# Optimization experiments

Hardware: AMD Instinct MI355X
Metric: run time of the kernel (lower is better)

The kernel has to match this reference:

```python
import jax, jax.numpy as jnp
import numpy as np

N, E, G = 100000, 1600000, 64
IN, H, OUT = 128, 64, 16  # hidden/2 = 32
SLOPE = 0.01


def setup_inputs() -> dict:
    key = jax.random.key(0)
    ks = jax.random.split(key, 7)
    features = jax.random.normal(ks[0], (N, IN), dtype=jnp.float32)
    src = jax.random.randint(ks[1], (E,), 0, N)
    dst = jax.random.randint(ks[2], (E,), 0, N)
    graph_ids = jnp.sort(jax.random.randint(ks[3], (N,), 0, G))
    # kaiming-uniform-ish fan_in init, bias=False everywhere
    W1 = jax.random.uniform(ks[4], (IN, H), jnp.float32, -1.0, 1.0) * np.sqrt(3.0 / IN)
    W2 = jax.random.uniform(ks[5], (H, H // 2), jnp.float32, -1.0, 1.0) * np.sqrt(3.0 / H)
    Wc = jax.random.uniform(ks[6], (H // 2, OUT), jnp.float32, -1.0, 1.0) * np.sqrt(3.0 / (H // 2))
    return {"features": features, "src": src, "dst": dst, "graph_ids": graph_ids,
            "W1": W1, "W2": W2, "Wc": Wc}


def _graph_conv(x, W, src, dst, n):
    # DGL GraphConv, norm='both', bias=False:
    # out = D_in^{-1/2} A (D_out^{-1/2} x) W   (degrees clamped to >= 1)
    ones = jnp.ones(src.shape[0], dtype=x.dtype)
    outdeg = jnp.clip(jax.ops.segment_sum(ones, src, num_segments=n), 1.0)
    indeg = jnp.clip(jax.ops.segment_sum(ones, dst, num_segments=n), 1.0)
    h = (x * jax.lax.rsqrt(outdeg)[:, None]) @ W  # project first (in_dim > out_dim)
    m = jax.ops.segment_sum(h[src], dst, num_segments=n)  # sparse aggregation
    return m * jax.lax.rsqrt(indeg)[:, None]


def reference(features, src, dst, graph_ids, W1, W2, Wc):
    h = jax.nn.leaky_relu(_graph_conv(features, W1, src, dst, N), SLOPE)
    h = jax.nn.leaky_relu(_graph_conv(h, W2, src, dst, N), SLOPE)
    # dropout is identity at inference
    sums = jax.ops.segment_sum(h, graph_ids, num_segments=G)
    cnts = jnp.clip(jax.ops.segment_sum(jnp.ones((N,), h.dtype), graph_ids, num_segments=G), 1.0)
    mean = sums / cnts[:, None]  # dgl.mean_nodes
    return mean @ Wc  # [G, OUT]
```

## Files before the change

kernel.cpp:

```cpp
#include <hip/hip_runtime.h>

#define NN 100000
#define NE 1600000
#define NG 64
#define D_IN 128
#define D_H 64
#define D_H2 32
#define D_OUT 16
#define SLOPE 0.01f
#define REC 48

#define BSH 9
#define NBK 196
#define NCB 500
#define CHE (NE / NCB)
#define PCAP 56

typedef _Float16 half2v __attribute__((ext_vector_type(2)));
typedef _Float16 h8 __attribute__((ext_vector_type(8)));
typedef float f32x4 __attribute__((ext_vector_type(4)));

__global__ __launch_bounds__(256) void p12_scatter(const int* __restrict__ src,
                                                   const int* __restrict__ dst,
                                                   unsigned* __restrict__ pkD,
                                                   unsigned short* __restrict__ pkS,
                                                   int* __restrict__ cntD,
                                                   int* __restrict__ cntS) {
  __shared__ int cD[NBK], cS[NBK];
  int b = blockIdx.x, t = threadIdx.x;
  for (int i = t; i < NBK; i += 256) { cD[i] = 0; cS[i] = 0; }
  __syncthreads();
  const int4* s4 = (const int4*)(src + b * CHE);
  const int4* d4 = (const int4*)(dst + b * CHE);
  for (int i = t; i < CHE / 4; i += 256) {
    int4 s = s4[i], d = d4[i];
#pragma unroll
    for (int j = 0; j < 4; ++j) {
      int ss = (j == 0) ? s.x : (j == 1) ? s.y : (j == 2) ? s.z : s.w;
      int dd = (j == 0) ? d.x : (j == 1) ? d.y : (j == 2) ? d.z : d.w;
      int kd = dd >> BSH;
      int pd = atomicAdd(&cD[kd], 1);
      if (pd < PCAP) pkD[((size_t)kd * NCB + b) * PCAP + pd] =
          ((unsigned)(dd & 511) << 17) | (unsigned)ss;
      int ks = ss >> BSH;
      int ps = atomicAdd(&cS[ks], 1);
      if (ps < PCAP) pkS[((size_t)ks * NCB + b) * PCAP + ps] =
          (unsigned short)(ss & 511);
    }
  }
  __syncthreads();
  for (int i = t; i < NBK; i += 256) {
    cntD[i * NCB + b] = min(cD[i], PCAP);
    cntS[i * NCB + b] = min(cS[i], PCAP);
  }
}

__global__ __launch_bounds__(256) void p3_build(const unsigned* __restrict__ pkD,
                                                const unsigned short* __restrict__ pkS,
                                                const int* __restrict__ cntD,
                                                const int* __restrict__ cntS,
                                                int* __restrict__ adj,
                                                int* __restrict__ indeg,
                                                int* __restrict__ outdeg) {
  __shared__ int hh[512];
  int bb = blockIdx.x, t = threadIdx.x;
  for (int i = t; i < 512; i += 256) hh[i] = 0;
  __syncthreads();
  if (bb < NBK) {
    int k = bb;
    int n0 = k << BSH;
    for (int s = t; s < NCB; s += 256) {
      int cnt = cntD[k * NCB + s];
      const uint4* r4 = (const uint4*)(pkD + ((size_t)k * NCB + s) * PCAP);
      for (int i = 0; i * 4 < cnt; ++i) {
        uint4 v = r4[i];
#pragma unroll
        for (int j = 0; j < 4; ++j) {
          int idx = i * 4 + j;
          if (idx < cnt) {
            unsigned rec = (j == 0) ? v.x : (j == 1) ? v.y : (j == 2) ? v.z : v.w;
            int local = rec >> 17;
            int pos = atomicAdd(&hh[local], 1);
            if (pos < REC) adj[(size_t)(n0 + local) * REC + pos] = (int)(rec & 0x1FFFF);
          }
        }
      }
    }
    __syncthreads();
    int4 ph = make_int4(NN, NN, NN, NN);
    for (int i = t; i < 512; i += 256) {
      int n = n0 + i;
      if (n < NN) {
        int dg = hh[i];
        indeg[n] = dg;
        int d = min(dg, REC);
        int dr = min((d + 7) & ~7, REC);
        int j = d;
        for (; j & 3; ++j) if (j < dr) adj[(size_t)n * REC + j] = NN;
        for (; j + 4 <= dr; j += 4) *(int4*)&adj[(size_t)n * REC + j] = ph;
      }
    }
  } else {
    int k = bb - NBK;
    for (int s = t; s < NCB; s += 256) {
      int cnt = cntS[k * NCB + s];
      const uint4* r4 = (const uint4*)(pkS + ((size_t)k * NCB + s) * PCAP);
      for (int i = 0; i * 8 < cnt; ++i) {
        uint4 v = r4[i];
        const unsigned short* u = (const unsigned short*)&v;
#pragma unroll
        for (int j = 0; j < 8; ++j) {
          int idx = i * 8 + j;
          if (idx < cnt) atomicAdd(&hh[u[j]], 1);
        }
      }
    }
    __syncthreads();
    int n0 = k << BSH;
    for (int i = t; i < 512; i += 256) {
      int n = n0 + i;
      if (n < NN) outdeg[n] = hh[i];
    }
  }
}

__global__ __launch_bounds__(256) void k_mm1f(const float* __restrict__ X,
                                              const float* __restrict__ W,
                                              const int* __restrict__ odeg,
                                              _Float16* __restrict__ Y) {
  __shared__ _Float16 Wt[64][136];
  int t = threadIdx.x;
  if (blockIdx.x == 0 && t < 64) Y[(size_t)NN * 64 + t] = (_Float16)0.f;
  for (int i = t; i < 128 * 64; i += 256) {
    int k = i >> 6, f = i & 63;
    Wt[f][k] = (_Float16)W[i];
  }
  __syncthreads();
  int lane = t & 63, w = t >> 6;
  int m = lane & 15, q = lane >> 4;
  h8 bf[4][4];
#pragma unroll
  for (int kc = 0; kc < 4; ++kc)
#pragma unroll
    for (int nt = 0; nt < 4; ++nt)
      bf[kc][nt] = *(const h8*)&Wt[nt * 16 + m][kc * 32 + q * 8];

  const int NT = NN / 16;
  int idx = blockIdx.x * 4 + w;
  int t0 = idx * 2, t1 = t0 + 1;
  f32x4 r0[8], r1[8];
  if (t0 < NT) {
    const f32x4* X0 = (const f32x4*)(X + (size_t)(t0 * 16 + m) * 128);
#pragma unroll
    for (int kc = 0; kc < 4; ++kc) {
      r0[kc * 2 + 0] = X0[kc * 8 + q * 2 + 0];
      r0[kc * 2 + 1] = X0[kc * 8 + q * 2 + 1];
    }
  }
  if (t1 < NT) {
    const f32x4* X1 = (const f32x4*)(X + (size_t)(t1 * 16 + m) * 128);
#pragma unroll
    for (int kc = 0; kc < 4; ++kc) {
      r1[kc * 2 + 0] = X1[kc * 8 + q * 2 + 0];
      r1[kc * 2 + 1] = X1[kc * 8 + q * 2 + 1];
    }
  }
#pragma unroll
  for (int half = 0; half < 2; ++half) {
    int tile = (half == 0) ? t0 : t1;
    if (tile >= NT) continue;
    f32x4* rr = (half == 0) ? r0 : r1;
    f32x4 acc[4] = {{0,0,0,0},{0,0,0,0},{0,0,0,0},{0,0,0,0}};
#pragma unroll
    for (int kc = 0; kc < 4; ++kc) {
      f32x4 x0 = rr[kc * 2 + 0], x1 = rr[kc * 2 + 1];
      h8 a;
      a[0] = (_Float16)x0.x; a[1] = (_Float16)x0.y;
      a[2] = (_Float16)x0.z; a[3] = (_Float16)x0.w;
      a[4] = (_Float16)x1.x; a[5] = (_Float16)x1.y;
      a[6] = (_Float16)x1.z; a[7] = (_Float16)x1.w;
#pragma unroll
      for (int nt = 0; nt < 4; ++nt)
        acc[nt] = __builtin_amdgcn_mfma_f32_16x16x32_f16(a, bf[kc][nt], acc[nt], 0, 0, 0);
    }
    int n0 = tile * 16;
#pragma unroll
    for (int reg = 0; reg < 4; ++reg) {
      int nn = n0 + q * 4 + reg;
      float sc = rsqrtf((float)max(odeg[nn], 1));
#pragma unroll
      for (int nt = 0; nt < 4; ++nt)
        Y[(size_t)nn * 64 + nt * 16 + m] = (_Float16)(acc[nt][reg] * sc);
    }
  }
}

__global__ __launch_bounds__(256) void k_aggmm2(const int* __restrict__ adj,
                                                const int* __restrict__ indeg,
                                                const int* __restrict__ odeg,
                                                const h8* __restrict__ H8,
                                                const float* __restrict__ W,
                                                _Float16* __restrict__ Y) {
  __shared__ int Adj[32][REC];
  __shared__ int Deg[32];
  __shared__ _Float16 Ht[32][72];
  __shared__ _Float16 Wt[32][72];
  int t = threadIdx.x;
  if (blockIdx.x == 0 && t < 32) Y[(size_t)NN * 32 + t] = (_Float16)0.f;
  for (int i = t; i < 64 * 32; i += 256) {
    int k = i >> 5, f = i & 31;
    Wt[f][k] = (_Float16)W[i];
  }
  int node0 = blockIdx.x * 32;
  {
    const int4* gadj = (const int4*)(adj + (size_t)node0 * REC);
    for (int i = t; i < 32 * (REC / 4); i += 256)
      ((int4*)Adj)[i] = gadj[i];
    if (t < 32) Deg[t] = indeg[node0 + t];
  }
  __syncthreads();
  int l8 = t & 7;
  int nd = t >> 3;
  int deg = Deg[nd];
  int groups = (min(deg, REC) + 7) >> 3;
  float acc[8] = {0.f, 0.f, 0.f, 0.f, 0.f, 0.f, 0.f, 0.f};
  for (int g = 0; g < groups; ++g) {
    int4 ca = *(const int4*)&Adj[nd][g * 8 + 0];
    int4 cb = *(const int4*)&Adj[nd][g * 8 + 4];
    h8 v0 = H8[(size_t)ca.x * 8 + l8];
    h8 v1 = H8[(size_t)ca.y * 8 + l8];
    h8 v2 = H8[(size_t)ca.z * 8 + l8];
    h8 v3 = H8[(size_t)ca.w * 8 + l8];
    h8 v4 = H8[(size_t)cb.x * 8 + l8];
    h8 v5 = H8[(size_t)cb.y * 8 + l8];
    h8 v6 = H8[(size_t)cb.z * 8 + l8];
    h8 v7 = H8[(size_t)cb.w * 8 + l8];
#pragma unroll
    for (int j = 0; j < 8; ++j)
      acc[j] += (((float)v0[j] + (float)v1[j]) + ((float)v2[j] + (float)v3[j])) +
                (((float)v4[j] + (float)v5[j]) + ((float)v6[j] + (float)v7[j]));
  }
  float sc = rsqrtf((float)max(deg, 1));
  h8 hv;
#pragma unroll
  for (int j = 0; j < 8; ++j) {
    float x = acc[j] * sc;
    hv[j] = (_Float16)((x > 0.f) ? x : SLOPE * x);
  }
  *(h8*)&Ht[nd][l8 * 8] = hv;
  __syncthreads();
  int lane = t & 63, w = t >> 6;
  if (w < 2) {
    int m = lane & 15, q = lane >> 4;
    h8 bf[2][2];
#pragma unroll
    for (int kc = 0; kc < 2; ++kc)
#pragma unroll
      for (int nt = 0; nt < 2; ++nt)
        bf[kc][nt] = *(const h8*)&Wt[nt * 16 + m][kc * 32 + q * 8];
    h8 af[2];
#pragma unroll
    for (int kc = 0; kc < 2; ++kc)
      af[kc] = *(const h8*)&Ht[w * 16 + m][kc * 32 + q * 8];
    f32x4 acc2[2] = {{0, 0, 0, 0}, {0, 0, 0, 0}};
#pragma unroll
    for (int kc = 0; kc < 2; ++kc)
#pragma unroll
      for (int nt = 0; nt < 2; ++nt)
        acc2[nt] = __builtin_amdgcn_mfma_f32_16x16x32_f16(af[kc], bf[kc][nt], acc2[nt], 0, 0, 0);
#pragma unroll
    for (int reg = 0; reg < 4; ++reg) {
      int nn = blockIdx.x * 32 + w * 16 + q * 4 + reg;
      float sco = rsqrtf((float)max(odeg[nn], 1));
#pragma unroll
      for (int nt = 0; nt < 2; ++nt)
        Y[(size_t)nn * 32 + nt * 16 + m] = (_Float16)(acc2[nt][reg] * sco);
    }
  }
}

__global__ __launch_bounds__(256) void k_agg32p(const int* __restrict__ adj,
                                                const int* __restrict__ indeg,
                                                const int* __restrict__ gid,
                                                const h8* __restrict__ H8,
                                                float* __restrict__ pool) {
  __shared__ int Adj2[64][REC];
  __shared__ int Deg2[64];
  __shared__ float lp[4][D_H2];
  __shared__ int gmin_s;
  int t = threadIdx.x;
  int l4 = t & 3;
  int nd = t >> 2;
  int node0 = blockIdx.x * 64;
  int node = node0 + nd;
  bool valid = node < NN;
  if (t == 0) gmin_s = gid[node0];
  for (int i = t; i < 4 * D_H2; i += 256) ((float*)lp)[i] = 0.f;
  {
    int maxi = (min(NN - node0, 64)) * (REC / 4);
    const int4* gadj = (const int4*)(adj + (size_t)node0 * REC);
    for (int i = t; i < 64 * (REC / 4); i += 256)
      ((int4*)Adj2)[i] = (i < maxi) ? gadj[i] : make_int4(NN, NN, NN, NN);
    if (t < 64) Deg2[t] = (node0 + t < NN) ? indeg[node0 + t] : 0;
  }
  __syncthreads();
  int deg = Deg2[nd];
  int groups = (min(deg, REC) + 7) >> 3;
  float acc[8] = {0.f, 0.f, 0.f, 0.f, 0.f, 0.f, 0.f, 0.f};
  for (int g = 0; g < groups; ++g) {
    int4 ca = *(const int4*)&Adj2[nd][g * 8 + 0];
    int4 cb = *(const int4*)&Adj2[nd][g * 8 + 4];
    h8 v0 = H8[(size_t)ca.x * 4 + l4];
    h8 v1 = H8[(size_t)ca.y * 4 + l4];
    h8 v2 = H8[(size_t)ca.z * 4 + l4];
    h8 v3 = H8[(size_t)ca.w * 4 + l4];
    h8 v4 = H8[(size_t)cb.x * 4 + l4];
    h8 v5 = H8[(size_t)cb.y * 4 + l4];
    h8 v6 = H8[(size_t)cb.z * 4 + l4];
    h8 v7 = H8[(size_t)cb.w * 4 + l4];
#pragma unroll
    for (int j = 0; j < 8; ++j)
      acc[j] += (((float)v0[j] + (float)v1[j]) + ((float)v2[j] + (float)v3[j])) +
                (((float)v4[j] + (float)v5[j]) + ((float)v6[j] + (float)v7[j]));
  }
  if (valid) {
    float sc = rsqrtf((float)max(deg, 1));
    int gl = min(gid[node] - gmin_s, 3);
#pragma unroll
    for (int j = 0; j < 8; ++j) {
      float x = acc[j] * sc;
      x = (x > 0.f) ? x : SLOPE * x;
      atomicAdd(&lp[gl][l4 * 8 + j], x);
    }
  }
  __syncthreads();
  if (t < 4 * D_H2) {
    float v = ((float*)lp)[t];
    if (v != 0.f) {
      int gl = t >> 5, f = t & 31;
      atomicAdd(&pool[(gmin_s + gl) * D_H2 + f], v);
    }
  }
}

__global__ __launch_bounds__(256) void k_out(const float* __restrict__ pool,
                                             const int* __restrict__ gid,
                                             const float* __restrict__ Wc,
                                             float* __restrict__ out) {
  __shared__ int bnd[NG + 1];
  __shared__ float mean[NG][D_H2];
  int t = threadIdx.x;
  if (t <= NG) {
    int target = t;
    int lo = 0, hi = NN;
    while (lo < hi) {
      int mid = (lo + hi) >> 1;
      if (gid[mid] < target) lo = mid + 1; else hi = mid;
    }
    bnd[t] = lo;
  }
  __syncthreads();
  for (int i = t; i < NG * D_H2; i += 256) {
    int g = i >> 5;
    float inv = 1.0f / (float)max(bnd[g + 1] - bnd[g], 1);
    ((float*)mean)[i] = pool[i] * inv;
  }
  __syncthreads();
  for (int i = t; i < NG * D_OUT; i += 256) {
    int g = i / D_OUT, o = i % D_OUT;
    float s = 0.f;
#pragma unroll
    for (int c = 0; c < D_H2; ++c) s += mean[g][c] * Wc[c * D_OUT + o];
    out[i] = s;
  }
}

extern "C" void kernel_launch(void* const* d_in, const int* in_sizes, int n_in,
                              void* d_out, int out_size, void* d_ws, size_t ws_size,
                              hipStream_t stream) {
  const float* X  = (const float*)d_in[0];
  const int*   src = (const int*)d_in[1];
  const int*   dst = (const int*)d_in[2];
  const int*   gid = (const int*)d_in[3];
  const float* W1 = (const float*)d_in[4];
  const float* W2 = (const float*)d_in[5];
  const float* Wc = (const float*)d_in[6];
  float* out = (float*)d_out;

  char* p = (char*)d_ws;
  auto alloc = [&](size_t bytes) {
    char* q = p;
    p += (bytes + 255) & ~(size_t)255;
    return q;
  };
  float*          pool   = (float*)alloc(NG * D_H2 * 4);
  int*            outdeg = (int*)alloc(NN * 4);
  int*            indeg  = (int*)alloc(NN * 4);
  int*            cntD   = (int*)alloc((size_t)NBK * NCB * 4);
  int*            cntS   = (int*)alloc((size_t)NBK * NCB * 4);
  unsigned*       pkD    = (unsigned*)alloc((size_t)NBK * NCB * PCAP * 4);
  unsigned short* pkS    = (unsigned short*)alloc((size_t)NBK * NCB * PCAP * 2);
  int*            adj    = (int*)alloc((size_t)NN * REC * 4);
  _Float16*       bufA   = (_Float16*)alloc((size_t)(NN + 1) * 64 * 2);
  _Float16*       bufC   = (_Float16*)alloc((size_t)(NN + 1) * 32 * 2);

  hipMemsetAsync(pool, 0, NG * D_H2 * 4, stream);

  p12_scatter<<<NCB, 256, 0, stream>>>(src, dst, pkD, pkS, cntD, cntS);
  p3_build<<<2 * NBK, 256, 0, stream>>>(pkD, pkS, cntD, cntS, adj, indeg, outdeg);

  k_mm1f<<<782, 256, 0, stream>>>(X, W1, outdeg, bufA);
  k_aggmm2<<<NN / 32, 256, 0, stream>>>(adj, indeg, outdeg, (const h8*)bufA, W2, bufC);
  k_agg32p<<<(NN + 63) / 64, 256, 0, stream>>>(adj, indeg, gid, (const h8*)bufC, pool);
  k_out<<<1, 256, 0, stream>>>(pool, gid, Wc, out);
}
```

Before: 218.4 us.

## Widen graph-build blocks, fold pool memset into scatter, unroll gathers by 16

Doubles the block size of the scatter and adjacency-build kernels so each thread handles one chunk or node directly. The separate pool memset is removed and the zeroing is done inside the scatter kernel's first block. Both aggregation kernels now gather 16 neighbours per iteration instead of 8, so more loads are in flight, and adjacency rows are padded to multiples of 16 to match. The cost is more registers per thread in the gather loops and extra padding writes for low-degree nodes.

Result: no change. 219.0 us (+0.3%).

```diff
diff --git a/kernel.cpp b/kernel.cpp
--- a/kernel.cpp
+++ b/kernel.cpp
@@ -20,19 +20,23 @@
 typedef _Float16 h8 __attribute__((ext_vector_type(8)));
 typedef float f32x4 __attribute__((ext_vector_type(4)));
 
-__global__ __launch_bounds__(256) void p12_scatter(const int* __restrict__ src,
+__global__ __launch_bounds__(512) void p12_scatter(const int* __restrict__ src,
                                                    const int* __restrict__ dst,
                                                    unsigned* __restrict__ pkD,
                                                    unsigned short* __restrict__ pkS,
                                                    int* __restrict__ cntD,
-                                                   int* __restrict__ cntS) {
+                                                   int* __restrict__ cntS,
+                                                   float* __restrict__ pool) {
   __shared__ int cD[NBK], cS[NBK];
   int b = blockIdx.x, t = threadIdx.x;
-  for (int i = t; i < NBK; i += 256) { cD[i] = 0; cS[i] = 0; }
+  if (b == 0) {
+    for (int i = t; i < NG * D_H2; i += 512) pool[i] = 0.f;
+  }
+  for (int i = t; i < NBK; i += 512) { cD[i] = 0; cS[i] = 0; }
   __syncthreads();
   const int4* s4 = (const int4*)(src + b * CHE);
   const int4* d4 = (const int4*)(dst + b * CHE);
-  for (int i = t; i < CHE / 4; i += 256) {
+  for (int i = t; i < CHE / 4; i += 512) {
     int4 s = s4[i], d = d4[i];
 #pragma unroll
     for (int j = 0; j < 4; ++j) {
@@ -49,13 +53,13 @@
     }
   }
   __syncthreads();
-  for (int i = t; i < NBK; i += 256) {
+  for (int i = t; i < NBK; i += 512) {
     cntD[i * NCB + b] = min(cD[i], PCAP);
     cntS[i * NCB + b] = min(cS[i], PCAP);
   }
 }
 
-__global__ __launch_bounds__(256) void p3_build(const unsigned* __restrict__ pkD,
+__global__ __launch_bounds__(512) void p3_build(const unsigned* __restrict__ pkD,
                                                 const unsigned short* __restrict__ pkS,
                                                 const int* __restrict__ cntD,
                                                 const int* __restrict__ cntS,
@@ -64,14 +68,14 @@
                                                 int* __restrict__ outdeg) {
   __shared__ int hh[512];
   int bb = blockIdx.x, t = threadIdx.x;
-  for (int i = t; i < 512; i += 256) hh[i] = 0;
+  hh[t] = 0;
   __syncthreads();
   if (bb < NBK) {
     int k = bb;
     int n0 = k << BSH;
-    for (int s = t; s < NCB; s += 256) {
-      int cnt = cntD[k * NCB + s];
-      const uint4* r4 = (const uint4*)(pkD + ((size_t)k * NCB + s) * PCAP);
+    if (t < NCB) {
+      int cnt = cntD[k * NCB + t];
+      const uint4* r4 = (const uint4*)(pkD + ((size_t)k * NCB + t) * PCAP);
       for (int i = 0; i * 4 < cnt; ++i) {
         uint4 v = r4[i];
 #pragma unroll
@@ -88,13 +92,13 @@
     }
     __syncthreads();
     int4 ph = make_int4(NN, NN, NN, NN);
-    for (int i = t; i < 512; i += 256) {
-      int n = n0 + i;
+    {
+      int n = n0 + t;
       if (n < NN) {
-        int dg = hh[i];
+        int dg = hh[t];
         indeg[n] = dg;
         int d = min(dg, REC);
-        int dr = min((d + 7) & ~7, REC);
+        int dr = min((d + 15) & ~15, REC);
         int j = d;
         for (; j & 3; ++j) if (j < dr) adj[(size_t)n * REC + j] = NN;
         for (; j + 4 <= dr; j += 4) *(int4*)&adj[(size_t)n * REC + j] = ph;
@@ -102,9 +106,9 @@
     }
   } else {
     int k = bb - NBK;
-    for (int s = t; s < NCB; s += 256) {
-      int cnt = cntS[k * NCB + s];
-      const uint4* r4 = (const uint4*)(pkS + ((size_t)k * NCB + s) * PCAP);
+    if (t < NCB) {
+      int cnt = cntS[k * NCB + t];
+      const uint4* r4 = (const uint4*)(pkS + ((size_t)k * NCB + t) * PCAP);
       for (int i = 0; i * 8 < cnt; ++i) {
         uint4 v = r4[i];
         const unsigned short* u = (const unsigned short*)&v;
@@ -117,10 +121,8 @@
     }
     __syncthreads();
     int n0 = k << BSH;
-    for (int i = t; i < 512; i += 256) {
-      int n = n0 + i;
-      if (n < NN) outdeg[n] = hh[i];
-    }
+    int n = n0 + t;
+    if (n < NN) outdeg[n] = hh[t];
   }
 }
 
@@ -222,23 +224,35 @@
   int l8 = t & 7;
   int nd = t >> 3;
   int deg = Deg[nd];
-  int groups = (min(deg, REC) + 7) >> 3;
+  int groups = (min(deg, REC) + 15) >> 4;
   float acc[8] = {0.f, 0.f, 0.f, 0.f, 0.f, 0.f, 0.f, 0.f};
   for (int g = 0; g < groups; ++g) {
-    int4 ca = *(const int4*)&Adj[nd][g * 8 + 0];
-    int4 cb = *(const int4*)&Adj[nd][g * 8 + 4];
-    h8 v0 = H8[(size_t)ca.x * 8 + l8];
-    h8 v1 = H8[(size_t)ca.y * 8 + l8];
-    h8 v2 = H8[(size_t)ca.z * 8 + l8];
-    h8 v3 = H8[(size_t)ca.w * 8 + l8];
-    h8 v4 = H8[(size_t)cb.x * 8 + l8];
-    h8 v5 = H8[(size_t)cb.y * 8 + l8];
-    h8 v6 = H8[(size_t)cb.z * 8 + l8];
-    h8 v7 = H8[(size_t)cb.w * 8 + l8];
+    int4 c0 = *(const int4*)&Adj[nd][g * 16 + 0];
+    int4 c1 = *(const int4*)&Adj[nd][g * 16 + 4];
+    int4 c2 = *(const int4*)&Adj[nd][g * 16 + 8];
+    int4 c3 = *(const int4*)&Adj[nd][g * 16 + 12];
+    h8 v0 = H8[(size_t)c0.x * 8 + l8];
+    h8 v1 = H8[(size_t)c0.y * 8 + l8];
+    h8 v2 = H8[(size_t)c0.z * 8 + l8];
+    h8 v3 = H8[(size_t)c0.w * 8 + l8];
+    h8 v4 = H8[(size_t)c1.x * 8 + l8];
+    h8 v5 = H8[(size_t)c1.y * 8 + l8];
+    h8 v6 = H8[(size_t)c1.z * 8 + l8];
+    h8 v7 = H8[(size_t)c1.w * 8 + l8];
+    h8 v8 = H8[(size_t)c2.x * 8 + l8];
+    h8 v9 = H8[(size_t)c2.y * 8 + l8];
+    h8 va = H8[(size_t)c2.z * 8 + l8];
+    h8 vb = H8[(size_t)c2.w * 8 + l8];
+    h8 vc = H8[(size_t)c3.x * 8 + l8];
+    h8 vd = H8[(size_t)c3.y * 8 + l8];
+    h8 ve = H8[(size_t)c3.z * 8 + l8];
+    h8 vf = H8[(size_t)c3.w * 8 + l8];
 #pragma unroll
     for (int j = 0; j < 8; ++j)
-      acc[j] += (((float)v0[j] + (float)v1[j]) + ((float)v2[j] + (float)v3[j])) +
-                (((float)v4[j] + (float)v5[j]) + ((float)v6[j] + (float)v7[j]));
+      acc[j] += ((((float)v0[j] + (float)v1[j]) + ((float)v2[j] + (float)v3[j])) +
+                 (((float)v4[j] + (float)v5[j]) + ((float)v6[j] + (float)v7[j]))) +
+                ((((float)v8[j] + (float)v9[j]) + ((float)va[j] + (float)vb[j])) +
+                 (((float)vc[j] + (float)vd[j]) + ((float)ve[j] + (float)vf[j])));
   }
   float sc = rsqrtf((float)max(deg, 1));
   h8 hv;
@@ -305,23 +319,35 @@
   }
   __syncthreads();
   int deg = Deg2[nd];
-  int groups = (min(deg, REC) + 7) >> 3;
+  int groups = (min(deg, REC) + 15) >> 4;
   float acc[8] = {0.f, 0.f, 0.f, 0.f, 0.f, 0.f, 0.f, 0.f};
   for (int g = 0; g < groups; ++g) {
-    int4 ca = *(const int4*)&Adj2[nd][g * 8 + 0];
-    int4 cb = *(const int4*)&Adj2[nd][g * 8 + 4];
-    h8 v0 = H8[(size_t)ca.x * 4 + l4];
-    h8 v1 = H8[(size_t)ca.y * 4 + l4];
-    h8 v2 = H8[(size_t)ca.z * 4 + l4];
-    h8 v3 = H8[(size_t)ca.w * 4 + l4];
-    h8 v4 = H8[(size_t)cb.x * 4 + l4];
-    h8 v5 = H8[(size_t)cb.y * 4 + l4];
-    h8 v6 = H8[(size_t)cb.z * 4 + l4];
-    h8 v7 = H8[(size_t)cb.w * 4 + l4];
+    int4 c0 = *(const int4*)&Adj2[nd][g * 16 + 0];
+    int4 c1 = *(const int4*)&Adj2[nd][g * 16 + 4];
+    int4 c2 = *(const int4*)&Adj2[nd][g * 16 + 8];
+    int4 c3 = *(const int4*)&Adj2[nd][g * 16 + 12];
+    h8 v0 = H8[(size_t)c0.x * 4 + l4];
+    h8 v1 = H8[(size_t)c0.y * 4 + l4];
+    h8 v2 = H8[(size_t)c0.z * 4 + l4];
+    h8 v3 = H8[(size_t)c0.w * 4 + l4];
+    h8 v4 = H8[(size_t)c1.x * 4 + l4];
+    h8 v5 = H8[(size_t)c1.y * 4 + l4];
+    h8 v6 = H8[(size_t)c1.z * 4 + l4];
+    h8 v7 = H8[(size_t)c1.w * 4 + l4];
+    h8 v8 = H8[(size_t)c2.x * 4 + l4];
+    h8 v9 = H8[(size_t)c2.y * 4 + l4];
+    h8 va = H8[(size_t)c2.z * 4 + l4];
+    h8 vb = H8[(size_t)c2.w * 4 + l4];
+    h8 vc = H8[(size_t)c3.x * 4 + l4];
+    h8 vd = H8[(size_t)c3.y * 4 + l4];
+    h8 ve = H8[(size_t)c3.z * 4 + l4];
+    h8 vf = H8[(size_t)c3.w * 4 + l4];
 #pragma unroll
     for (int j = 0; j < 8; ++j)
-      acc[j] += (((float)v0[j] + (float)v1[j]) + ((float)v2[j] + (float)v3[j])) +
-                (((float)v4[j] + (float)v5[j]) + ((float)v6[j] + (float)v7[j]));
+      acc[j] += ((((float)v0[j] + (float)v1[j]) + ((float)v2[j] + (float)v3[j])) +
+                 (((float)v4[j] + (float)v5[j]) + ((float)v6[j] + (float)v7[j]))) +
+                ((((float)v8[j] + (float)v9[j]) + ((float)va[j] + (float)vb[j])) +
+                 (((float)vc[j] + (float)vd[j]) + ((float)ve[j] + (float)vf[j])));
   }
   if (valid) {
     float sc = rsqrtf((float)max(deg, 1));
@@ -404,10 +430,8 @@
   _Float16*       bufA   = (_Float16*)alloc((size_t)(NN + 1) * 64 * 2);
   _Float16*       bufC   = (_Float16*)alloc((size_t)(NN + 1) * 32 * 2);
 
-  hipMemsetAsync(pool, 0, NG * D_H2 * 4, stream);
-
-  p12_scatter<<<NCB, 256, 0, stream>>>(src, dst, pkD, pkS, cntD, cntS);
-  p3_build<<<2 * NBK, 256, 0, stream>>>(pkD, pkS, cntD, cntS, adj, indeg, outdeg);
+  p12_scatter<<<NCB, 512, 0, stream>>>(src, dst, pkD, pkS, cntD, cntS, pool);
+  p3_build<<<2 * NBK, 512, 0, stream>>>(pkD, pkS, cntD, cntS, adj, indeg, outdeg);
 
   k_mm1f<<<782, 256, 0, stream>>>(X, W1, outdeg, bufA);
   k_aggmm2<<<NN / 32, 256, 0, stream>>>(adj, indeg, outdeg, (const h8*)bufA, W2, bufC);
```
